# Optimization experiments

Measured on AMD Instinct MI355X. Metric: run time of the kernel, lower is better.

## Reference

```python
import jax, jax.numpy as jnp
import numpy as np

CHUNK = 256  # hard-coded chunk size in the original parallel_scan (state resets each chunk)


def setup_inputs() -> dict:
    key = jax.random.key(0)
    ks = jax.random.split(key, 8)
    d_model, d_inner, n_state, dt_rank, k = 1024, 2048, 16, 64, 3
    B, L = 2, 1024
    s = 0.02  # init scale for linear weights
    return {
        "x": jax.random.normal(ks[0], (B, L, d_model), jnp.float32),
        "W_in": jax.random.normal(ks[1], (2 * d_inner, d_model), jnp.float32) * s,
        "b_in": jnp.zeros((2 * d_inner,), jnp.float32),
        "conv_w": jax.random.normal(ks[2], (d_inner, 1, k), jnp.float32) * s,
        "conv_b": jnp.zeros((d_inner,), jnp.float32),
        "W_x": jax.random.normal(ks[3], (dt_rank + 2 * n_state, d_inner), jnp.float32) * s,
        "W_dt": jax.random.normal(ks[4], (d_inner, dt_rank), jnp.float32) * s,
        "b_dt": jnp.zeros((d_inner,), jnp.float32),
        "A_log": jax.random.normal(ks[5], (d_inner, n_state), jnp.float32),
        "W_out": jax.random.normal(ks[6], (d_model, d_inner), jnp.float32) * s,
        "b_out": jnp.zeros((d_model,), jnp.float32),
    }


def reference(x, W_in, b_in, conv_w, conv_b, W_x, W_dt, b_dt, A_log, W_out, b_out):
    Bsz, L, _ = x.shape
    d_inner, n_state = A_log.shape
    dt_rank = W_dt.shape[1]
    k = conv_w.shape[-1]

    # in_proj then split into x-branch and residual gate branch
    xr = x @ W_in.T + b_in                       # (B, L, 2*D)
    xc, res = jnp.split(xr, 2, axis=-1)          # each (B, L, D)

    # depthwise causal conv1d (torch pads k-1 both sides then truncates to L == left-pad k-1)
    h = jnp.transpose(xc, (0, 2, 1))             # (B, D, L)
    h = jax.lax.conv_general_dilated(
        h, conv_w, window_strides=(1,), padding=[(k - 1, 0)],
        dimension_numbers=("NCH", "OIH", "NCH"), feature_group_count=d_inner)
    h = h + conv_b[None, :, None]
    u = jax.nn.silu(jnp.transpose(h, (0, 2, 1)))  # (B, L, D)

    # x_proj -> delta_low_rank, B, C
    xp = u @ W_x.T                                # (B, L, dt_rank + 2N)
    dlt, Bm, Cm = jnp.split(xp, [dt_rank, dt_rank + n_state], axis=-1)
    delta = jax.nn.softplus(dlt @ W_dt.T + b_dt)  # (B, L, D)

    A = -jnp.exp(A_log)                           # (D, N), negative
    dA = jnp.exp(jnp.einsum('bld,dn->bldn', delta, A))      # (B, L, D, N), in (0,1]
    dBu = jnp.einsum('bld,bln,bld->bldn', delta, Bm, u)     # (B, L, D, N)

    # chunked scan: state resets to 0 at the start of each CHUNK (faithful to original)
    nc = L // CHUNK
    dA_c = dA.reshape(Bsz, nc, CHUNK, d_inner, n_state).transpose(2, 0, 1, 3, 4)
    dBu_c = dBu.reshape(Bsz, nc, CHUNK, d_inner, n_state).transpose(2, 0, 1, 3, 4)
    C_c = Cm.reshape(Bsz, nc, CHUNK, n_state).transpose(2, 0, 1, 3)

    def step(carry, inp):
        a, bu, c = inp                             # (B, nc, D, N), (B, nc, D, N), (B, nc, N)
        carry = a * carry + bu
        y = jnp.einsum('bkdn,bkn->bkd', carry, c)
        return carry, y

    init = jnp.zeros((Bsz, nc, d_inner, n_state), x.dtype)
    _, ys = jax.lax.scan(step, init, (dA_c, dBu_c, C_c))   # ys: (CHUNK, B, nc, D)
    y = ys.transpose(1, 2, 0, 3).reshape(Bsz, L, d_inner)

    y = y * jax.nn.silu(res)
    return y @ W_out.T + b_out
```

## Files before the change

### kernel.cpp

```cpp
#include <hip/hip_runtime.h>
#include <stdint.h>
#include <stddef.h>

typedef __attribute__((ext_vector_type(8))) short short8;
typedef __attribute__((ext_vector_type(4))) float floatx4;
typedef unsigned short ushort_t;

__device__ __forceinline__ ushort_t f2bf(float f) {
    union { float f; uint32_t u; } v; v.f = f;
    return (ushort_t)((v.u + 0x7fffu + ((v.u >> 16) & 1u)) >> 16);
}
__device__ __forceinline__ float bf2f(ushort_t u) {
    union { uint32_t u; float f; } v; v.u = ((uint32_t)u) << 16; return v.f;
}

__device__ __forceinline__ void load16_lds(const ushort_t* g, short* l) {
    __builtin_amdgcn_global_load_lds((const __attribute__((address_space(1))) void*)g,
                                     (__attribute__((address_space(3))) void*)l, 16, 0, 0);
}

enum { EPI_SPLIT = 0, EPI_SOFTPLUS = 1, EPI_OUT = 2, EPI_PARTIAL = 3 };

__global__ __launch_bounds__(256)
void cvt5(const float* __restrict__ x, const float* __restrict__ win,
          const float* __restrict__ wx, const float* __restrict__ wdt,
          const float* __restrict__ wout,
          ushort_t* __restrict__ xb, ushort_t* __restrict__ winb,
          ushort_t* __restrict__ wxb, ushort_t* __restrict__ wdtb,
          ushort_t* __restrict__ woutb)
{
    int g = blockIdx.x * 256 + threadIdx.x;
    const float* s; ushort_t* d; int off;
    if      (g < 524288)  { s = x;    d = xb;    off = g; }
    else if (g < 1572864) { s = win;  d = winb;  off = g - 524288; }
    else if (g < 1622016) { s = wx;   d = wxb;   off = g - 1572864; }
    else if (g < 1654784) { s = wdt;  d = wdtb;  off = g - 1622016; }
    else                  { s = wout; d = woutb; off = g - 1654784; }
    float4 v = reinterpret_cast<const float4*>(s)[off];
    union { ushort_t u[4]; uint2 q; } o;
    o.u[0] = f2bf(v.x); o.u[1] = f2bf(v.y); o.u[2] = f2bf(v.z); o.u[3] = f2bf(v.w);
    *reinterpret_cast<uint2*>(d + (size_t)off * 4) = o.q;
}

template<int BM, int BN, int BK, int WR, int WC, int EPI>
__global__ __launch_bounds__(256)
void gemm_bt(const ushort_t* __restrict__ A, int lda,
             const ushort_t* __restrict__ Bw, int ldb,
             float* __restrict__ out0, float* __restrict__ out1,
             ushort_t* __restrict__ outb,
             const float* __restrict__ bias,
             int N, int kchunk)
{
    constexpr int TM = BM / WR / 16;
    constexpr int TN = BN / WC / 16;
    static_assert(BM % (WR * 16) == 0 && BN % (WC * 16) == 0, "tile");
    static_assert((BM * BK) % 2048 == 0 && (BN * BK) % 2048 == 0, "stage");

    __shared__ __align__(16) short As[BM * BK];
    __shared__ __align__(16) short Bs[BN * BK];

    const int tid  = threadIdx.x;
    const int m0   = blockIdx.x * BM;
    const int n0   = blockIdx.y * BN;
    const int ks   = blockIdx.z;
    const int kbeg = ks * kchunk;

    const int w    = tid >> 6;
    const int lane = tid & 63;
    const int quad = lane >> 4;
    const int l16  = lane & 15;
    const int wr   = w / WC, wc = w % WC;
    const int wm   = wr * (BM / WR);
    const int wn   = wc * (BN / WC);

    floatx4 acc[TM][TN];
#pragma unroll
    for (int i = 0; i < TM; i++)
#pragma unroll
        for (int j = 0; j < TN; j++) acc[i][j] = (floatx4){0.f, 0.f, 0.f, 0.f};

    constexpr int nA = BM * BK / 2048;
    constexpr int nB = BN * BK / 2048;
    constexpr int CPR = BK / 8;

    for (int kb = kbeg; kb < kbeg + kchunk; kb += BK) {
        __syncthreads();
#pragma unroll
        for (int i = 0; i < nA; i++) {
            int c = i * 256 + tid;
            int r = c / CPR, kc = (c % CPR) * 8;
            load16_lds(A + (size_t)(m0 + r) * lda + kb + kc, &As[r * BK + kc]);
        }
#pragma unroll
        for (int i = 0; i < nB; i++) {
            int c = i * 256 + tid;
            int r = c / CPR, kc = (c % CPR) * 8;
            load16_lds(Bw + (size_t)(n0 + r) * ldb + kb + kc, &Bs[r * BK + kc]);
        }
        __syncthreads();
#pragma unroll
        for (int kk = 0; kk < BK / 32; kk++) {
            short8 af[TM], bfr[TN];
#pragma unroll
            for (int t = 0; t < TM; t++)
                af[t] = *reinterpret_cast<const short8*>(&As[(wm + t * 16 + l16) * BK + kk * 32 + quad * 8]);
#pragma unroll
            for (int u2 = 0; u2 < TN; u2++)
                bfr[u2] = *reinterpret_cast<const short8*>(&Bs[(wn + u2 * 16 + l16) * BK + kk * 32 + quad * 8]);
#pragma unroll
            for (int t = 0; t < TM; t++)
#pragma unroll
                for (int u2 = 0; u2 < TN; u2++)
                    acc[t][u2] = __builtin_amdgcn_mfma_f32_16x16x32_bf16(af[t], bfr[u2], acc[t][u2], 0, 0, 0);
        }
    }

#pragma unroll
    for (int t = 0; t < TM; t++) {
#pragma unroll
        for (int u2 = 0; u2 < TN; u2++) {
#pragma unroll
            for (int r = 0; r < 4; r++) {
                int row = m0 + wm + t * 16 + quad * 4 + r;
                int col = n0 + wn + u2 * 16 + l16;
                float val = acc[t][u2][r];
                if (EPI == EPI_SPLIT) {
                    val += bias[col];
                    if (col < 2048) {
                        out0[(size_t)row * 2048 + col] = val;
                    } else {
                        float sr = val / (1.f + __expf(-val));
                        outb[(size_t)row * 2048 + col - 2048] = f2bf(sr);
                    }
                } else if (EPI == EPI_SOFTPLUS) {
                    val += bias[col];
                    float sp = fmaxf(val, 0.f) + __logf(1.f + __expf(-fabsf(val)));
                    out0[(size_t)row * N + col] = sp;
                } else if (EPI == EPI_OUT) {
                    val += bias[col];
                    out0[(size_t)row * N + col] = val;
                } else {
                    out0[((size_t)ks * 2048 + row) * 96 + col] = val;
                }
            }
        }
    }
}

__global__ __launch_bounds__(256)
void conv_silu(const float* __restrict__ xc, const float* __restrict__ cw,
               const float* __restrict__ cb, ushort_t* __restrict__ ub)
{
    int id = blockIdx.x * 256 + threadIdx.x;
    int m  = id >> 9;
    int d4 = (id & 511) * 4;
    int l  = m & 1023;

    const float4 zero = make_float4(0.f, 0.f, 0.f, 0.f);
    float4 a = *reinterpret_cast<const float4*>(xc + (size_t)m * 2048 + d4);
    float4 b = (l >= 1) ? *reinterpret_cast<const float4*>(xc + (size_t)(m - 1) * 2048 + d4) : zero;
    float4 c = (l >= 2) ? *reinterpret_cast<const float4*>(xc + (size_t)(m - 2) * 2048 + d4) : zero;

    float av[4] = {a.x, a.y, a.z, a.w};
    float bv[4] = {b.x, b.y, b.z, b.w};
    float cv[4] = {c.x, c.y, c.z, c.w};
    union { ushort_t u[4]; uint2 q; } o;
#pragma unroll
    for (int j = 0; j < 4; j++) {
        int d = d4 + j;
        float v = cb[d] + cw[d * 3 + 0] * cv[j] + cw[d * 3 + 1] * bv[j] + cw[d * 3 + 2] * av[j];
        o.u[j] = f2bf(v / (1.f + __expf(-v)));
    }
    *reinterpret_cast<uint2*>(ub + (size_t)m * 2048 + d4) = o.q;
}

__global__ __launch_bounds__(256)
void xp_reduce(const float* __restrict__ part, float* __restrict__ xp, ushort_t* __restrict__ dltb)
{
    int e = blockIdx.x * 256 + threadIdx.x;
    float s = 0.f;
#pragma unroll
    for (int ks = 0; ks < 4; ks++) s += part[(size_t)ks * 2048 * 96 + e];
    xp[e] = s;
    int n = e % 96, m = e / 96;
    if (n < 64) dltb[(size_t)m * 64 + n] = f2bf(s);
}

__global__ __launch_bounds__(1024, 8)
void scan_kernel(const float* __restrict__ delta, const ushort_t* __restrict__ ub,
                 const float* __restrict__ xp, const float* __restrict__ A_log,
                 const ushort_t* __restrict__ sgb, ushort_t* __restrict__ ygb)
{
    __shared__ __align__(16) float Bsh[256 * 16];
    __shared__ __align__(16) float Csh[256 * 16];
    __shared__ float sQ[16][32][17];
    __shared__ float sS[16][32];

    const int tid  = threadIdx.x;
    const int w    = tid >> 6;
    const int lane = tid & 63;
    const int dl   = lane & 31;
    const int h    = lane >> 5;
    const int d    = blockIdx.x * 32 + dl;
    const int c    = blockIdx.y;
    const int mbase = (c >> 2) * 1024 + (c & 3) * 256;

    {
        int r = tid >> 2, part = tid & 3;
        const float4* rp = reinterpret_cast<const float4*>(xp + (size_t)(mbase + r) * 96 + 64);
        reinterpret_cast<float4*>(Bsh + r * 16)[part] = rp[part];
        reinterpret_cast<float4*>(Csh + r * 16)[part] = rp[part + 4];
    }

    float Av[8];
    {
        const float4* ap = reinterpret_cast<const float4*>(A_log + (size_t)d * 16 + h * 8);
        float4 a0 = ap[0], a1 = ap[1];
        Av[0] = -__expf(a0.x); Av[1] = -__expf(a0.y); Av[2] = -__expf(a0.z); Av[3] = -__expf(a0.w);
        Av[4] = -__expf(a1.x); Av[5] = -__expf(a1.y); Av[6] = -__expf(a1.z); Av[7] = -__expf(a1.w);
    }

    float s[8];
#pragma unroll
    for (int n = 0; n < 8; n++) s[n] = 0.f;
    float sumdv = 0.f;
    const int t0 = w * 16;
    __syncthreads();

#pragma unroll 4
    for (int tt = 0; tt < 16; tt++) {
        int t = t0 + tt;
        size_t idx = (size_t)(mbase + t) * 2048 + d;
        float dvv = delta[idx];
        float uv  = bf2f(ub[idx]);
        float dvu = dvv * uv;
        sumdv += dvv;
        const float* Brow = &Bsh[t * 16 + h * 8];
#pragma unroll
        for (int n = 0; n < 8; n++) {
            float dA = __expf(dvv * Av[n]);
            s[n] = fmaf(dA, s[n], dvu * Brow[n]);
        }
    }
#pragma unroll
    for (int n = 0; n < 8; n++) sQ[w][dl][h * 8 + n] = s[n];
    if (h == 0) sS[w][dl] = sumdv;
    __syncthreads();

    {
        float sin_[8];
#pragma unroll
        for (int n = 0; n < 8; n++) sin_[n] = 0.f;
        float cum = 0.f;
        for (int v = w - 1; v >= 0; v--) {
#pragma unroll
            for (int n = 0; n < 8; n++)
                sin_[n] += __expf(Av[n] * cum) * sQ[v][dl][h * 8 + n];
            cum += sS[v][dl];
        }
#pragma unroll
        for (int n = 0; n < 8; n++) s[n] = sin_[n];
    }

#pragma unroll 2
    for (int tt = 0; tt < 16; tt++) {
        int t = t0 + tt;
        size_t idx = (size_t)(mbase + t) * 2048 + d;
        float dvv = delta[idx];
        float uv  = bf2f(ub[idx]);
        float dvu = dvv * uv;
        const float* Brow = &Bsh[t * 16 + h * 8];
        const float* Crow = &Csh[t * 16 + h * 8];
        float y = 0.f;
#pragma unroll
        for (int n = 0; n < 8; n++) {
            float dA = __expf(dvv * Av[n]);
            s[n] = fmaf(dA, s[n], dvu * Brow[n]);
            y = fmaf(s[n], Crow[n], y);
        }
        y += __shfl_xor(y, 32);
        if (h == 0) {
            float sr = bf2f(sgb[idx]);
            ygb[idx] = f2bf(y * sr);
        }
    }
}

extern "C" void kernel_launch(void* const* d_in, const int* in_sizes, int n_in,
                              void* d_out, int out_size, void* d_ws, size_t ws_size,
                              hipStream_t stream)
{
    const float* x      = (const float*)d_in[0];
    const float* W_in   = (const float*)d_in[1];
    const float* b_in   = (const float*)d_in[2];
    const float* conv_w = (const float*)d_in[3];
    const float* conv_b = (const float*)d_in[4];
    const float* W_x    = (const float*)d_in[5];
    const float* W_dt   = (const float*)d_in[6];
    const float* b_dt   = (const float*)d_in[7];
    const float* A_log  = (const float*)d_in[8];
    const float* W_out  = (const float*)d_in[9];
    const float* b_out  = (const float*)d_in[10];
    float* out = (float*)d_out;

    char* p = (char*)d_ws;
    auto alloc = [&](size_t bytes) { char* r = p; p += (bytes + 255) & ~(size_t)255; return r; };
    ushort_t* xbf    = (ushort_t*)alloc(2048ull * 1024 * 2);
    ushort_t* winbf  = (ushort_t*)alloc(4096ull * 1024 * 2);
    ushort_t* wxbf   = (ushort_t*)alloc(96ull * 2048 * 2);
    ushort_t* wdtbf  = (ushort_t*)alloc(2048ull * 64 * 2);
    ushort_t* woutbf = (ushort_t*)alloc(1024ull * 2048 * 2);
    float*    xc     = (float*)alloc(2048ull * 2048 * 4);
    ushort_t* sgb    = (ushort_t*)alloc(2048ull * 2048 * 2);
    ushort_t* ub     = (ushort_t*)alloc(2048ull * 2048 * 2);
    float*    xpp    = (float*)alloc(4ull * 2048 * 96 * 4);
    float*    xp     = (float*)alloc(2048ull * 96 * 4);
    ushort_t* dltb   = (ushort_t*)alloc(2048ull * 64 * 2);
    ushort_t* ygb    = (ushort_t*)alloc(2048ull * 2048 * 2);
    float*    delta  = xc;

    cvt5<<<8512, 256, 0, stream>>>(x, W_in, W_x, W_dt, W_out,
                                   xbf, winbf, wxbf, wdtbf, woutbf);

    gemm_bt<128, 128, 64, 2, 2, EPI_SPLIT><<<dim3(16, 32), 256, 0, stream>>>(
        xbf, 1024, winbf, 1024, xc, nullptr, sgb, b_in, 4096, 1024);

    conv_silu<<<4096, 256, 0, stream>>>(xc, conv_w, conv_b, ub);

    gemm_bt<64, 96, 64, 4, 1, EPI_PARTIAL><<<dim3(32, 1, 4), 256, 0, stream>>>(
        ub, 2048, wxbf, 2048, xpp, nullptr, nullptr, nullptr, 96, 512);

    xp_reduce<<<768, 256, 0, stream>>>(xpp, xp, dltb);

    gemm_bt<64, 64, 64, 2, 2, EPI_SOFTPLUS><<<dim3(32, 32), 256, 0, stream>>>(
        dltb, 64, wdtbf, 64, delta, nullptr, nullptr, b_dt, 2048, 64);

    scan_kernel<<<dim3(64, 8), 1024, 0, stream>>>(delta, ub, xp, A_log, sgb, ygb);

    gemm_bt<128, 64, 64, 2, 2, EPI_OUT><<<dim3(16, 16), 256, 0, stream>>>(
        ygb, 2048, woutbf, 2048, out, nullptr, nullptr, b_out, 1024, 2048);
}
```

Before: 236.5 us.

## Store conv input as bf16, deepen x_proj split-K, single-pass scan with carry correction

The in-proj epilogue now writes the conv branch as bf16 instead of fp32, halving that intermediate's traffic, and conv_silu reads bf16. The x_proj GEMM uses 8 K-splits instead of 4 for more parallelism, with the reduce summing 8 partials. The scan no longer re-reads delta/u in a second pass: it keeps local outputs and cumulative delta in registers, then adds the inter-segment state contribution via exp(A*cum). The output GEMM uses smaller 64x64 tiles for more blocks. The changes add bf16 rounding of pre-conv activations and raise register pressure in the scan.

```diff
diff --git a/kernel.cpp b/kernel.cpp
--- a/kernel.cpp
+++ b/kernel.cpp
@@ -46,8 +46,9 @@
 __global__ __launch_bounds__(256)
 void gemm_bt(const ushort_t* __restrict__ A, int lda,
              const ushort_t* __restrict__ Bw, int ldb,
-             float* __restrict__ out0, float* __restrict__ out1,
-             ushort_t* __restrict__ outb,
+             float* __restrict__ out0,
+             ushort_t* __restrict__ outg,
+             ushort_t* __restrict__ outc,
              const float* __restrict__ bias,
              int N, int kchunk)
 {
@@ -127,10 +128,10 @@
                 if (EPI == EPI_SPLIT) {
                     val += bias[col];
                     if (col < 2048) {
-                        out0[(size_t)row * 2048 + col] = val;
+                        outc[(size_t)row * 2048 + col] = f2bf(val);
                     } else {
                         float sr = val / (1.f + __expf(-val));
-                        outb[(size_t)row * 2048 + col - 2048] = f2bf(sr);
+                        outg[(size_t)row * 2048 + col - 2048] = f2bf(sr);
                     }
                 } else if (EPI == EPI_SOFTPLUS) {
                     val += bias[col];
@@ -148,7 +149,7 @@
 }
 
 __global__ __launch_bounds__(256)
-void conv_silu(const float* __restrict__ xc, const float* __restrict__ cw,
+void conv_silu(const ushort_t* __restrict__ xc, const float* __restrict__ cw,
                const float* __restrict__ cb, ushort_t* __restrict__ ub)
 {
     int id = blockIdx.x * 256 + threadIdx.x;
@@ -156,19 +157,19 @@
     int d4 = (id & 511) * 4;
     int l  = m & 1023;
 
-    const float4 zero = make_float4(0.f, 0.f, 0.f, 0.f);
-    float4 a = *reinterpret_cast<const float4*>(xc + (size_t)m * 2048 + d4);
-    float4 b = (l >= 1) ? *reinterpret_cast<const float4*>(xc + (size_t)(m - 1) * 2048 + d4) : zero;
-    float4 c = (l >= 2) ? *reinterpret_cast<const float4*>(xc + (size_t)(m - 2) * 2048 + d4) : zero;
-
-    float av[4] = {a.x, a.y, a.z, a.w};
-    float bv[4] = {b.x, b.y, b.z, b.w};
-    float cv[4] = {c.x, c.y, c.z, c.w};
+    union { uint2 q; ushort_t u[4]; } a, b, c;
+    a.q = *reinterpret_cast<const uint2*>(xc + (size_t)m * 2048 + d4);
+    if (l >= 1) b.q = *reinterpret_cast<const uint2*>(xc + (size_t)(m - 1) * 2048 + d4);
+    else        { b.q.x = 0; b.q.y = 0; }
+    if (l >= 2) c.q = *reinterpret_cast<const uint2*>(xc + (size_t)(m - 2) * 2048 + d4);
+    else        { c.q.x = 0; c.q.y = 0; }
+
     union { ushort_t u[4]; uint2 q; } o;
 #pragma unroll
     for (int j = 0; j < 4; j++) {
         int d = d4 + j;
-        float v = cb[d] + cw[d * 3 + 0] * cv[j] + cw[d * 3 + 1] * bv[j] + cw[d * 3 + 2] * av[j];
+        float v = cb[d] + cw[d * 3 + 0] * bf2f(c.u[j]) + cw[d * 3 + 1] * bf2f(b.u[j])
+                        + cw[d * 3 + 2] * bf2f(a.u[j]);
         o.u[j] = f2bf(v / (1.f + __expf(-v)));
     }
     *reinterpret_cast<uint2*>(ub + (size_t)m * 2048 + d4) = o.q;
@@ -180,7 +181,7 @@
     int e = blockIdx.x * 256 + threadIdx.x;
     float s = 0.f;
 #pragma unroll
-    for (int ks = 0; ks < 4; ks++) s += part[(size_t)ks * 2048 * 96 + e];
+    for (int ks = 0; ks < 8; ks++) s += part[(size_t)ks * 2048 * 96 + e];
     xp[e] = s;
     int n = e % 96, m = e / 96;
     if (n < 64) dltb[(size_t)m * 64 + n] = f2bf(s);
@@ -223,52 +224,20 @@
     float s[8];
 #pragma unroll
     for (int n = 0; n < 8; n++) s[n] = 0.f;
-    float sumdv = 0.f;
+    float yl[16], cd[16];
+    float cum = 0.f;
     const int t0 = w * 16;
     __syncthreads();
 
-#pragma unroll 4
+#pragma unroll
     for (int tt = 0; tt < 16; tt++) {
         int t = t0 + tt;
         size_t idx = (size_t)(mbase + t) * 2048 + d;
         float dvv = delta[idx];
         float uv  = bf2f(ub[idx]);
         float dvu = dvv * uv;
-        sumdv += dvv;
-        const float* Brow = &Bsh[t * 16 + h * 8];
-#pragma unroll
-        for (int n = 0; n < 8; n++) {
-            float dA = __expf(dvv * Av[n]);
-            s[n] = fmaf(dA, s[n], dvu * Brow[n]);
-        }
-    }
-#pragma unroll
-    for (int n = 0; n < 8; n++) sQ[w][dl][h * 8 + n] = s[n];
-    if (h == 0) sS[w][dl] = sumdv;
-    __syncthreads();
-
-    {
-        float sin_[8];
-#pragma unroll
-        for (int n = 0; n < 8; n++) sin_[n] = 0.f;
-        float cum = 0.f;
-        for (int v = w - 1; v >= 0; v--) {
-#pragma unroll
-            for (int n = 0; n < 8; n++)
-                sin_[n] += __expf(Av[n] * cum) * sQ[v][dl][h * 8 + n];
-            cum += sS[v][dl];
-        }
-#pragma unroll
-        for (int n = 0; n < 8; n++) s[n] = sin_[n];
-    }
-
-#pragma unroll 2
-    for (int tt = 0; tt < 16; tt++) {
-        int t = t0 + tt;
-        size_t idx = (size_t)(mbase + t) * 2048 + d;
-        float dvv = delta[idx];
-        float uv  = bf2f(ub[idx]);
-        float dvu = dvv * uv;
+        cum += dvv;
+        cd[tt] = cum;
         const float* Brow = &Bsh[t * 16 + h * 8];
         const float* Crow = &Csh[t * 16 + h * 8];
         float y = 0.f;
@@ -278,8 +247,39 @@
             s[n] = fmaf(dA, s[n], dvu * Brow[n]);
             y = fmaf(s[n], Crow[n], y);
         }
+        yl[tt] = y;
+    }
+#pragma unroll
+    for (int n = 0; n < 8; n++) sQ[w][dl][h * 8 + n] = s[n];
+    if (h == 0) sS[w][dl] = cum;
+    __syncthreads();
+
+    float sin_[8];
+#pragma unroll
+    for (int n = 0; n < 8; n++) sin_[n] = 0.f;
+    {
+        float cc = 0.f;
+        for (int v = w - 1; v >= 0; v--) {
+#pragma unroll
+            for (int n = 0; n < 8; n++)
+                sin_[n] += __expf(Av[n] * cc) * sQ[v][dl][h * 8 + n];
+            cc += sS[v][dl];
+        }
+    }
+
+#pragma unroll
+    for (int tt = 0; tt < 16; tt++) {
+        int t = t0 + tt;
+        float y = yl[tt];
+        if (w > 0) {
+            const float* Crow = &Csh[t * 16 + h * 8];
+#pragma unroll
+            for (int n = 0; n < 8; n++)
+                y = fmaf(__expf(Av[n] * cd[tt]) * sin_[n], Crow[n], y);
+        }
         y += __shfl_xor(y, 32);
         if (h == 0) {
+            size_t idx = (size_t)(mbase + t) * 2048 + d;
             float sr = bf2f(sgb[idx]);
             ygb[idx] = f2bf(y * sr);
         }
@@ -310,25 +310,26 @@
     ushort_t* wxbf   = (ushort_t*)alloc(96ull * 2048 * 2);
     ushort_t* wdtbf  = (ushort_t*)alloc(2048ull * 64 * 2);
     ushort_t* woutbf = (ushort_t*)alloc(1024ull * 2048 * 2);
-    float*    xc     = (float*)alloc(2048ull * 2048 * 4);
+    char*     slabS  = alloc(2048ull * 2048 * 4);
     ushort_t* sgb    = (ushort_t*)alloc(2048ull * 2048 * 2);
     ushort_t* ub     = (ushort_t*)alloc(2048ull * 2048 * 2);
-    float*    xpp    = (float*)alloc(4ull * 2048 * 96 * 4);
+    float*    xpp    = (float*)alloc(8ull * 2048 * 96 * 4);
     float*    xp     = (float*)alloc(2048ull * 96 * 4);
     ushort_t* dltb   = (ushort_t*)alloc(2048ull * 64 * 2);
     ushort_t* ygb    = (ushort_t*)alloc(2048ull * 2048 * 2);
-    float*    delta  = xc;
+    ushort_t* xcb    = (ushort_t*)slabS;
+    float*    delta  = (float*)slabS;
 
     cvt5<<<8512, 256, 0, stream>>>(x, W_in, W_x, W_dt, W_out,
                                    xbf, winbf, wxbf, wdtbf, woutbf);
 
     gemm_bt<128, 128, 64, 2, 2, EPI_SPLIT><<<dim3(16, 32), 256, 0, stream>>>(
-        xbf, 1024, winbf, 1024, xc, nullptr, sgb, b_in, 4096, 1024);
-
-    conv_silu<<<4096, 256, 0, stream>>>(xc, conv_w, conv_b, ub);
-
-    gemm_bt<64, 96, 64, 4, 1, EPI_PARTIAL><<<dim3(32, 1, 4), 256, 0, stream>>>(
-        ub, 2048, wxbf, 2048, xpp, nullptr, nullptr, nullptr, 96, 512);
+        xbf, 1024, winbf, 1024, nullptr, sgb, xcb, b_in, 4096, 1024);
+
+    conv_silu<<<4096, 256, 0, stream>>>(xcb, conv_w, conv_b, ub);
+
+    gemm_bt<64, 96, 64, 4, 1, EPI_PARTIAL><<<dim3(32, 1, 8), 256, 0, stream>>>(
+        ub, 2048, wxbf, 2048, xpp, nullptr, nullptr, nullptr, 96, 256);
 
     xp_reduce<<<768, 256, 0, stream>>>(xpp, xp, dltb);
 
@@ -337,6 +338,6 @@
 
     scan_kernel<<<dim3(64, 8), 1024, 0, stream>>>(delta, ub, xp, A_log, sgb, ygb);
 
-    gemm_bt<128, 64, 64, 2, 2, EPI_OUT><<<dim3(16, 16), 256, 0, stream>>>(
+    gemm_bt<64, 64, 64, 2, 2, EPI_OUT><<<dim3(32, 16), 256, 0, stream>>>(
         ygb, 2048, woutbf, 2048, out, nullptr, nullptr, b_out, 1024, 2048);
 }
```

After: 577.5 us. +144.2%, slower.
